# Kernel tuning notes

Hardware: AMD Instinct MI355X
Metric: run time of the kernel (lower is better)

Reference implementation:

```python
import jax, jax.numpy as jnp
import numpy as np
import math

# LLaMA-7B-style int8 attention (torch-int Int8LlamaAttention)
B, S, HID, NH, HD = 2, 1024, 4096, 32, 128
THETA = 10000.0
# per-tensor quantization scales (as produced by from_float)
S_IN, S_W, S_B = 0.02, 0.01, 0.1
S_Q, S_K, S_V, S_O = 0.05, 0.05, 0.05, 0.05


def _rope_tables(position_ids):
    inv_freq = 1.0 / (THETA ** (jnp.arange(0, HD, 2, dtype=jnp.float32) / HD))
    freqs = position_ids.astype(jnp.float32)[..., None] * inv_freq  # [B,S,HD//2]
    emb = jnp.concatenate([freqs, freqs], axis=-1)  # [B,S,HD]
    return jnp.cos(emb)[:, None], jnp.sin(emb)[:, None]  # [B,1,S,HD]


def _rotate_half(x):
    return jnp.concatenate([-x[..., HD // 2:], x[..., :HD // 2]], axis=-1)


def _quant_i8(x):
    return jnp.clip(jnp.round(x), -128, 127).astype(jnp.int8)


def _w8a8b8o8(x_i8, w_i8, b_i8, alpha, beta):
    # int8 GEMM with int32 accumulation, fused dequant-requant to int8
    acc = jnp.einsum('bsk,nk->bsn', x_i8.astype(jnp.int32), w_i8.astype(jnp.int32))
    return _quant_i8(acc.astype(jnp.float32) * alpha + b_i8.astype(jnp.float32) * beta)


def setup_inputs() -> dict:
    key = jax.random.key(0)
    ks = jax.random.split(key, 9)
    ri8 = lambda k, shp: jax.random.randint(k, shp, -127, 128, dtype=jnp.int8)
    return {
        'hidden_states': jax.random.normal(ks[0], (B, S, HID), jnp.float32),
        'position_ids': jnp.broadcast_to(jnp.arange(S, dtype=jnp.int32), (B, S)),
        'w_q': ri8(ks[1], (HID, HID)),
        'w_k': ri8(ks[2], (HID, HID)),
        'w_v': ri8(ks[3], (HID, HID)),
        'w_o': ri8(ks[4], (HID, HID)),
        'b_q': ri8(ks[5], (HID,)),
        'b_k': ri8(ks[6], (HID,)),
        'b_v': ri8(ks[7], (HID,)),
        'b_o': jax.random.normal(ks[8], (HID,), jnp.float32) * 0.01,
    }


def reference(hidden_states, position_ids, w_q, w_k, w_v, w_o, b_q, b_k, b_v, b_o):
    # quantize activations, run int8 q/k/v projections (W8A8B8O8Linear)
    x_i8 = _quant_i8(hidden_states / S_IN)
    q = _w8a8b8o8(x_i8, w_q, b_q, S_IN * S_W / S_Q, S_B / S_Q)
    k = _w8a8b8o8(x_i8, w_k, b_k, S_IN * S_W / S_K, S_B / S_K)
    v = _w8a8b8o8(x_i8, w_v, b_v, S_IN * S_W / S_V, S_B / S_V)
    to_heads = lambda t: t.reshape(B, S, NH, HD).transpose(0, 2, 1, 3)  # [B,NH,S,HD]
    q, k, v = to_heads(q), to_heads(k), to_heads(v)
    # RoPE applied on dequantized int8 values, requantized for the int8 qk bmm
    cos, sin = _rope_tables(position_ids)
    qf, kf = q.astype(jnp.float32), k.astype(jnp.float32)
    q_i8 = _quant_i8(qf * cos + _rotate_half(qf) * sin)
    k_i8 = _quant_i8(kf * cos + _rotate_half(kf) * sin)
    # BMM_S8T_S8N_F32T: int8 QK^T -> fp32 with scale s_q*s_k, then /sqrt(d)
    attn = jnp.einsum('bhsd,bhtd->bhst', q_i8.astype(jnp.int32), k_i8.astype(jnp.int32))
    attn = attn.astype(jnp.float32) * (S_Q * S_K) / math.sqrt(HD)
    # NOTE: source never applies the attention mask (`attn_weights = attn_weights`)
    p = jax.nn.softmax(attn, axis=-1)
    # probs quantized to int8 with scale 1/127 for BMM_S8T_S8N_S8T
    p_i8 = _quant_i8(p * 127.0)
    ctx = jnp.einsum('bhst,bhtd->bhsd', p_i8.astype(jnp.int32), v.astype(jnp.int32))
    ctx_i8 = _quant_i8(ctx.astype(jnp.float32) * ((1.0 / 127.0) * S_V / S_O))
    ctx_i8 = ctx_i8.transpose(0, 2, 1, 3).reshape(B, S, HID)
    # W8A8BFP32OFP32 o_proj: int8 GEMM, fp32 output + fp32 bias
    out = jnp.einsum('bsk,nk->bsn', ctx_i8.astype(jnp.int32), w_o.astype(jnp.int32))
    return out.astype(jnp.float32) * (S_O * S_W) + b_o
```

## Files before the change

### kernel.cpp

```cpp
#include <hip/hip_runtime.h>
#include <hip/hip_bf16.h>
#include <cstdint>
#include <cstddef>

typedef int v4i __attribute__((ext_vector_type(4)));

#define NH 32
#define HD 128
#define SEQ 1024
#define HID 4096
#define BB 2
#define BKB 128

__device__ __forceinline__ signed char quant_i8(float x) {
    float r = rintf(x);
    r = fminf(fmaxf(r, -128.0f), 127.0f);
    return (signed char)r;
}

#define GLOAD_LDS16(g, l) \
    __builtin_amdgcn_global_load_lds((const __attribute__((address_space(1))) void*)(g), \
                                     (__attribute__((address_space(3))) void*)(l), 16, 0, 0)

__global__ __launch_bounds__(256) void pack4_i8_kernel(
    const int* __restrict__ s0, const int* __restrict__ s1,
    const int* __restrict__ s2, const int* __restrict__ s3,
    signed char* __restrict__ d0, signed char* __restrict__ d1,
    signed char* __restrict__ d2, signed char* __restrict__ d3, int n4)
{
    int i = blockIdx.x * 256 + threadIdx.x;
    int which = i / n4;
    int idx = i - which * n4;
    const int* src = (which == 0) ? s0 : (which == 1) ? s1 : (which == 2) ? s2 : s3;
    signed char* dst = (which == 0) ? d0 : (which == 1) ? d1 : (which == 2) ? d2 : d3;
    int4 v = ((const int4*)src)[idx];
    char4 c;
    c.x = (signed char)v.x; c.y = (signed char)v.y;
    c.z = (signed char)v.z; c.w = (signed char)v.w;
    ((char4*)dst)[idx] = c;
}

__global__ __launch_bounds__(256) void quant_x_kernel(const float* __restrict__ src,
                                                      signed char* __restrict__ dst, int n4) {
    int i = blockIdx.x * 256 + threadIdx.x;
    if (i >= n4) return;
    float4 v = ((const float4*)src)[i];
    char4 c;
    c.x = quant_i8(v.x * 50.0f);
    c.y = quant_i8(v.y * 50.0f);
    c.z = quant_i8(v.z * 50.0f);
    c.w = quant_i8(v.w * 50.0f);
    ((char4*)dst)[i] = c;
}

template<int TM, bool F32OUT>
__device__ __forceinline__ void gemm_core(
    const signed char* __restrict__ A, const signed char* __restrict__ Bw,
    const void* __restrict__ bias, void* __restrict__ outp,
    int m0, int n0, int N, int K, float alpha, float beta)
{
    constexpr int MI = TM / 32;
    constexpr int PA = TM / 32;
    __shared__ __align__(16) signed char sA[TM * BKB];
    __shared__ __align__(16) signed char sB[128 * BKB];

    const int t    = threadIdx.x;
    const int w    = t >> 6;
    const int lane = t & 63;
    const int lm   = lane & 15;
    const int quad = lane >> 4;
    const int wm   = (w >> 1) * (TM / 2);
    const int wn   = (w & 1) * 64;

    int srowA[PA], skcA[PA];
    #pragma unroll
    for (int p = 0; p < PA; p++) {
        int si = t + 256 * p;
        int row = si >> 3;
        srowA[p] = row;
        skcA[p] = ((si & 7) - (row >> 1)) & 7;
    }
    int srowB[4], skcB[4];
    #pragma unroll
    for (int p = 0; p < 4; p++) {
        int si = t + 256 * p;
        int row = si >> 3;
        srowB[p] = row;
        skcB[p] = ((si & 7) - (row >> 1)) & 7;
    }

    v4i acc[MI][4] = {};

    for (int k0 = 0; k0 < K; k0 += BKB) {
        __syncthreads();
        #pragma unroll
        for (int p = 0; p < PA; p++) {
            const signed char* ga = A + (size_t)(m0 + srowA[p]) * K + k0 + skcA[p] * 16;
            GLOAD_LDS16(ga, sA + t * 16 + p * 4096);
        }
        #pragma unroll
        for (int p = 0; p < 4; p++) {
            const signed char* gb = Bw + (size_t)(n0 + srowB[p]) * K + k0 + skcB[p] * 16;
            GLOAD_LDS16(gb, sB + t * 16 + p * 4096);
        }
        __syncthreads();

        #pragma unroll
        for (int ks = 0; ks < 2; ks++) {
            v4i af[MI], bf[4];
            #pragma unroll
            for (int i = 0; i < MI; i++) {
                int row = wm + 16 * i + lm;
                int slot = (ks * 4 + quad + (lm >> 1)) & 7;
                af[i] = *(const v4i*)(sA + row * BKB + slot * 16);
            }
            #pragma unroll
            for (int j = 0; j < 4; j++) {
                int row = wn + 16 * j + lm;
                int slot = (ks * 4 + quad + (lm >> 1)) & 7;
                bf[j] = *(const v4i*)(sB + row * BKB + slot * 16);
            }
            #pragma unroll
            for (int i = 0; i < MI; i++)
                #pragma unroll
                for (int j = 0; j < 4; j++)
                    acc[i][j] = __builtin_amdgcn_mfma_i32_16x16x64_i8(af[i], bf[j], acc[i][j], 0, 0, 0);
        }
    }

    const int orow = quad * 4;
    #pragma unroll
    for (int i = 0; i < MI; i++) {
        #pragma unroll
        for (int j = 0; j < 4; j++) {
            #pragma unroll
            for (int r = 0; r < 4; r++) {
                int row = m0 + wm + 16 * i + orow + r;
                int col = n0 + wn + 16 * j + lm;
                float v = (float)acc[i][j][r];
                if (F32OUT) {
                    ((float*)outp)[(size_t)row * N + col] = v * alpha + ((const float*)bias)[col];
                } else {
                    float q = v * alpha + (float)((const int*)bias)[col] * beta;
                    ((signed char*)outp)[(size_t)row * N + col] = quant_i8(q);
                }
            }
        }
    }
}

__global__ __launch_bounds__(256) void gemm_qkv(
    const signed char* __restrict__ x8,
    const signed char* __restrict__ wq, const signed char* __restrict__ wk,
    const signed char* __restrict__ wv,
    const int* __restrict__ bq, const int* __restrict__ bk, const int* __restrict__ bv,
    signed char* __restrict__ q8, signed char* __restrict__ k8, signed char* __restrict__ v8)
{
    const int nblk = blockIdx.x;
    const int which = nblk >> 5;
    const int n0 = (nblk & 31) * 128;
    const int m0 = blockIdx.y * 128;
    const signed char* Bw = (which == 0) ? wq : (which == 1) ? wk : wv;
    const int* bias = (which == 0) ? bq : (which == 1) ? bk : bv;
    signed char* outp = (which == 0) ? q8 : (which == 1) ? k8 : v8;
    gemm_core<128, false>(x8, Bw, bias, outp, m0, n0, HID, HID, 0.004f, 2.0f);
}

__global__ __launch_bounds__(256) void gemm_o(
    const signed char* __restrict__ c8, const signed char* __restrict__ wo,
    const float* __restrict__ bo, float* __restrict__ outp)
{
    gemm_core<64, true>(c8, wo, bo, outp, blockIdx.y * 64, blockIdx.x * 128,
                        HID, HID, 0.0005f, 0.0f);
}

__global__ __launch_bounds__(128) void rope_kernel(
    const int* __restrict__ pos_ids, signed char* __restrict__ q,
    signed char* __restrict__ k, const signed char* __restrict__ v,
    signed char* __restrict__ vt)
{
    const int bid = blockIdx.x;
    const int sg = bid & 127;
    const int h  = (bid >> 7) & (NH - 1);
    const int b  = bid >> 12;
    const int d  = threadIdx.x;
    const int s0 = sg * 8;
    const int bh = b * NH + h;

    float inv = expf(-(float)(2 * (d & 63)) * (9.210340371976184f / 128.0f));

    float qd[8], qp[8], kd[8], kp[8];
    signed char vd[8];
    int pos[8];
    size_t base[8];
    #pragma unroll
    for (int i = 0; i < 8; i++) {
        int s = s0 + i;
        base[i] = ((size_t)(b * SEQ + s) * NH + h) * (size_t)HD;
        pos[i] = pos_ids[b * SEQ + s];
        qd[i] = (float)q[base[i] + d];
        qp[i] = (float)q[base[i] + (d ^ 64)];
        kd[i] = (float)k[base[i] + d];
        kp[i] = (float)k[base[i] + (d ^ 64)];
        vd[i] = v[base[i] + d];
    }
    __syncthreads();

    union { signed char c[8]; int2 i2; } vu;
    #pragma unroll
    for (int i = 0; i < 8; i++) {
        float freq = (float)pos[i] * inv;
        float cs = cosf(freq), sn = sinf(freq);
        float rotq = (d < 64) ? -qp[i] : qp[i];
        float rotk = (d < 64) ? -kp[i] : kp[i];
        q[base[i] + d] = quant_i8(qd[i] * cs + rotq * sn);
        k[base[i] + d] = quant_i8(kd[i] * cs + rotk * sn);
        vu.c[i] = vd[i];
    }
    *(int2*)(vt + ((size_t)(bh * HD + d)) * SEQ + s0) = vu.i2;
}

__global__ __launch_bounds__(256, 4) void attn_kernel(
    const signed char* __restrict__ q, const signed char* __restrict__ k,
    const signed char* __restrict__ vt, signed char* __restrict__ ctx)
{
    __shared__ __align__(16) signed char p8[16 * 1040];
    __shared__ float red[64];

    const int w    = threadIdx.x >> 6;
    const int lane = threadIdx.x & 63;
    const int bid  = blockIdx.x;
    const int mt   = bid & 63;
    const int bh   = bid >> 6;
    const int b    = bh >> 5, h = bh & 31;
    const int m0   = mt * 16;
    const int lm   = lane & 15;
    const int quad = lane >> 4;

    const float SCALE = 0.0025f / 11.313708498984761f;
    const float LOG2E = 1.4426950408889634f;

    const signed char* qbase = q + ((size_t)(b * SEQ + m0 + lm) * NH + h) * (size_t)HD + quad * 16;
    v4i qb0 = *(const v4i*)qbase;
    v4i qb1 = *(const v4i*)(qbase + 64);

    float vals[16][4];
    #pragma unroll
    for (int j = 0; j < 16; j++) {
        int t0 = w * 256 + j * 16;
        const signed char* kb = k + ((size_t)(b * SEQ + t0 + lm) * NH + h) * (size_t)HD + quad * 16;
        v4i a0 = *(const v4i*)kb;
        v4i a1 = *(const v4i*)(kb + 64);
        v4i acc = {};
        acc = __builtin_amdgcn_mfma_i32_16x16x64_i8(a0, qb0, acc, 0, 0, 0);
        acc = __builtin_amdgcn_mfma_i32_16x16x64_i8(a1, qb1, acc, 0, 0, 0);
        #pragma unroll
        for (int r = 0; r < 4; r++) vals[j][r] = (float)acc[r] * SCALE;
    }

    float mx = vals[0][0];
    #pragma unroll
    for (int j = 0; j < 16; j++)
        #pragma unroll
        for (int r = 0; r < 4; r++) mx = fmaxf(mx, vals[j][r]);
    mx = fmaxf(mx, __shfl_xor(mx, 16));
    mx = fmaxf(mx, __shfl_xor(mx, 32));
    if (lane < 16) red[w * 16 + lane] = mx;
    __syncthreads();
    mx = fmaxf(fmaxf(red[lm], red[16 + lm]), fmaxf(red[32 + lm], red[48 + lm]));

    float sum = 0.f;
    #pragma unroll
    for (int j = 0; j < 16; j++)
        #pragma unroll
        for (int r = 0; r < 4; r++) {
            vals[j][r] = exp2f((vals[j][r] - mx) * LOG2E);
            sum += vals[j][r];
        }
    sum += __shfl_xor(sum, 16);
    sum += __shfl_xor(sum, 32);
    __syncthreads();
    if (lane < 16) red[w * 16 + lane] = sum;
    __syncthreads();
    sum = (red[lm] + red[16 + lm]) + (red[32 + lm] + red[48 + lm]);
    float sf = 127.0f / sum;

    #pragma unroll
    for (int j = 0; j < 16; j++) {
        union { signed char cc[4]; int ii; } u;
        #pragma unroll
        for (int r = 0; r < 4; r++) u.cc[r] = quant_i8(vals[j][r] * sf);
        *(int*)(p8 + lm * 1040 + w * 256 + j * 16 + quad * 4) = u.ii;
    }
    __syncthreads();

    const int lkb = quad * 16;
    v4i accp[2] = {};
    for (int kk = 0; kk < SEQ; kk += 64) {
        v4i af = *(const v4i*)(p8 + lm * 1040 + kk + lkb);
        #pragma unroll
        for (int j = 0; j < 2; j++) {
            int col = w * 32 + j * 16;
            const signed char* vb = vt + ((size_t)(bh * HD + col + lm)) * (size_t)SEQ + kk + lkb;
            accp[j] = __builtin_amdgcn_mfma_i32_16x16x64_i8(af, *(const v4i*)vb, accp[j], 0, 0, 0);
        }
    }
    #pragma unroll
    for (int j = 0; j < 2; j++) {
        #pragma unroll
        for (int r = 0; r < 4; r++) {
            int row = quad * 4 + r;
            int col = w * 32 + j * 16 + lm;
            ctx[((size_t)(b * SEQ + m0 + row) * NH + h) * (size_t)HD + col] =
                quant_i8((float)accp[j][r] * (1.0f / 127.0f));
        }
    }
}

extern "C" void kernel_launch(void* const* d_in, const int* in_sizes, int n_in,
                              void* d_out, int out_size, void* d_ws, size_t ws_size,
                              hipStream_t stream)
{
    const float* hidden = (const float*)d_in[0];
    const int* pos_ids  = (const int*)d_in[1];
    const int* w_q = (const int*)d_in[2];
    const int* w_k = (const int*)d_in[3];
    const int* w_v = (const int*)d_in[4];
    const int* w_o = (const int*)d_in[5];
    const int* b_q = (const int*)d_in[6];
    const int* b_k = (const int*)d_in[7];
    const int* b_v = (const int*)d_in[8];
    const float* b_o = (const float*)d_in[9];
    float* out = (float*)d_out;

    char* ws = (char*)d_ws;
    const size_t WSZ = (size_t)HID * HID;
    signed char* wq8 = (signed char*)ws;
    signed char* wk8 = wq8 + WSZ;
    signed char* wv8 = wk8 + WSZ;
    signed char* wo8 = wv8 + WSZ;
    signed char* x8  = wo8 + WSZ;
    const size_t ASZ = (size_t)BB * SEQ * HID;
    signed char* q8  = x8 + ASZ;
    signed char* k8  = q8 + ASZ;
    signed char* v8  = k8 + ASZ;
    signed char* vt8 = v8 + ASZ;
    signed char* c8  = vt8 + ASZ;

    int wn4 = HID * HID / 4;
    pack4_i8_kernel<<<4 * wn4 / 256, 256, 0, stream>>>(w_q, w_k, w_v, w_o,
                                                       wq8, wk8, wv8, wo8, wn4);
    int xn4 = (int)(ASZ / 4);
    quant_x_kernel<<<xn4 / 256, 256, 0, stream>>>(hidden, x8, xn4);

    gemm_qkv<<<dim3(96, 16), 256, 0, stream>>>(x8, wq8, wk8, wv8, b_q, b_k, b_v,
                                               q8, k8, v8);

    rope_kernel<<<BB * NH * (SEQ / 8), 128, 0, stream>>>(pos_ids, q8, k8, v8, vt8);
    attn_kernel<<<BB * NH * (SEQ / 16), 256, 0, stream>>>(q8, k8, vt8, c8);

    gemm_o<<<dim3(32, 32), 256, 0, stream>>>(c8, wo8, b_o, out);
}
```

Baseline: 604.8 us.

## Double-buffer LDS in int8 GEMMs and process 32 query rows per attention block

```diff
diff --git a/kernel.cpp b/kernel.cpp
--- a/kernel.cpp
+++ b/kernel.cpp
@@ -53,84 +53,84 @@
     ((char4*)dst)[i] = c;
 }
 
-template<int TM, bool F32OUT>
-__device__ __forceinline__ void gemm_core(
+template<bool F32OUT>
+__device__ __forceinline__ void gemm_core_db(
     const signed char* __restrict__ A, const signed char* __restrict__ Bw,
     const void* __restrict__ bias, void* __restrict__ outp,
     int m0, int n0, int N, int K, float alpha, float beta)
 {
-    constexpr int MI = TM / 32;
-    constexpr int PA = TM / 32;
-    __shared__ __align__(16) signed char sA[TM * BKB];
-    __shared__ __align__(16) signed char sB[128 * BKB];
+    __shared__ __align__(16) signed char sA[2 * 128 * BKB];
+    __shared__ __align__(16) signed char sB[2 * 128 * BKB];
 
     const int t    = threadIdx.x;
     const int w    = t >> 6;
     const int lane = t & 63;
     const int lm   = lane & 15;
     const int quad = lane >> 4;
-    const int wm   = (w >> 1) * (TM / 2);
+    const int wm   = (w >> 1) * 64;
     const int wn   = (w & 1) * 64;
 
-    int srowA[PA], skcA[PA];
-    #pragma unroll
-    for (int p = 0; p < PA; p++) {
-        int si = t + 256 * p;
-        int row = si >> 3;
-        srowA[p] = row;
-        skcA[p] = ((si & 7) - (row >> 1)) & 7;
-    }
-    int srowB[4], skcB[4];
+    int srow[4], skc[4];
     #pragma unroll
     for (int p = 0; p < 4; p++) {
         int si = t + 256 * p;
         int row = si >> 3;
-        srowB[p] = row;
-        skcB[p] = ((si & 7) - (row >> 1)) & 7;
-    }
-
-    v4i acc[MI][4] = {};
-
+        srow[p] = row;
+        skc[p] = ((si & 7) - (row >> 1)) & 7;
+    }
+
+    v4i acc[4][4] = {};
+
+    #pragma unroll
+    for (int p = 0; p < 4; p++) {
+        GLOAD_LDS16(A  + (size_t)(m0 + srow[p]) * K + skc[p] * 16, sA + t * 16 + p * 4096);
+        GLOAD_LDS16(Bw + (size_t)(n0 + srow[p]) * K + skc[p] * 16, sB + t * 16 + p * 4096);
+    }
+
+    int buf = 0;
     for (int k0 = 0; k0 < K; k0 += BKB) {
         __syncthreads();
-        #pragma unroll
-        for (int p = 0; p < PA; p++) {
-            const signed char* ga = A + (size_t)(m0 + srowA[p]) * K + k0 + skcA[p] * 16;
-            GLOAD_LDS16(ga, sA + t * 16 + p * 4096);
-        }
-        #pragma unroll
-        for (int p = 0; p < 4; p++) {
-            const signed char* gb = Bw + (size_t)(n0 + srowB[p]) * K + k0 + skcB[p] * 16;
-            GLOAD_LDS16(gb, sB + t * 16 + p * 4096);
-        }
-        __syncthreads();
-
+
+        if (k0 + BKB < K) {
+            int nb = buf ^ 1;
+            #pragma unroll
+            for (int p = 0; p < 4; p++) {
+                GLOAD_LDS16(A  + (size_t)(m0 + srow[p]) * K + k0 + BKB + skc[p] * 16,
+                            sA + nb * 16384 + t * 16 + p * 4096);
+                GLOAD_LDS16(Bw + (size_t)(n0 + srow[p]) * K + k0 + BKB + skc[p] * 16,
+                            sB + nb * 16384 + t * 16 + p * 4096);
+            }
+        }
+
+        const signed char* pA = sA + buf * 16384;
+        const signed char* pB = sB + buf * 16384;
         #pragma unroll
         for (int ks = 0; ks < 2; ks++) {
-            v4i af[MI], bf[4];
-            #pragma unroll
-            for (int i = 0; i < MI; i++) {
+            v4i af[4], bf[4];
+            #pragma unroll
+            for (int i = 0; i < 4; i++) {
                 int row = wm + 16 * i + lm;
                 int slot = (ks * 4 + quad + (lm >> 1)) & 7;
-                af[i] = *(const v4i*)(sA + row * BKB + slot * 16);
+                af[i] = *(const v4i*)(pA + row * BKB + slot * 16);
             }
             #pragma unroll
             for (int j = 0; j < 4; j++) {
                 int row = wn + 16 * j + lm;
                 int slot = (ks * 4 + quad + (lm >> 1)) & 7;
-                bf[j] = *(const v4i*)(sB + row * BKB + slot * 16);
+                bf[j] = *(const v4i*)(pB + row * BKB + slot * 16);
             }
             #pragma unroll
-            for (int i = 0; i < MI; i++)
+            for (int i = 0; i < 4; i++)
                 #pragma unroll
                 for (int j = 0; j < 4; j++)
                     acc[i][j] = __builtin_amdgcn_mfma_i32_16x16x64_i8(af[i], bf[j], acc[i][j], 0, 0, 0);
         }
+        buf ^= 1;
     }
 
     const int orow = quad * 4;
     #pragma unroll
-    for (int i = 0; i < MI; i++) {
+    for (int i = 0; i < 4; i++) {
         #pragma unroll
         for (int j = 0; j < 4; j++) {
             #pragma unroll
@@ -163,15 +163,15 @@
     const signed char* Bw = (which == 0) ? wq : (which == 1) ? wk : wv;
     const int* bias = (which == 0) ? bq : (which == 1) ? bk : bv;
     signed char* outp = (which == 0) ? q8 : (which == 1) ? k8 : v8;
-    gemm_core<128, false>(x8, Bw, bias, outp, m0, n0, HID, HID, 0.004f, 2.0f);
+    gemm_core_db<false>(x8, Bw, bias, outp, m0, n0, HID, HID, 0.004f, 2.0f);
 }
 
 __global__ __launch_bounds__(256) void gemm_o(
     const signed char* __restrict__ c8, const signed char* __restrict__ wo,
     const float* __restrict__ bo, float* __restrict__ outp)
 {
-    gemm_core<64, true>(c8, wo, bo, outp, blockIdx.y * 64, blockIdx.x * 128,
-                        HID, HID, 0.0005f, 0.0f);
+    gemm_core_db<true>(c8, wo, bo, outp, blockIdx.y * 128, blockIdx.x * 128,
+                       HID, HID, 0.0005f, 0.0f);
 }
 
 __global__ __launch_bounds__(128) void rope_kernel(
@@ -220,89 +220,108 @@
     *(int2*)(vt + ((size_t)(bh * HD + d)) * SEQ + s0) = vu.i2;
 }
 
-__global__ __launch_bounds__(256, 4) void attn_kernel(
+__global__ __launch_bounds__(256) void attn_kernel(
     const signed char* __restrict__ q, const signed char* __restrict__ k,
     const signed char* __restrict__ vt, signed char* __restrict__ ctx)
 {
-    __shared__ __align__(16) signed char p8[16 * 1040];
-    __shared__ float red[64];
+    __shared__ __align__(16) signed char p8[32 * 1040];
+    __shared__ float red[128];
 
     const int w    = threadIdx.x >> 6;
     const int lane = threadIdx.x & 63;
     const int bid  = blockIdx.x;
-    const int mt   = bid & 63;
-    const int bh   = bid >> 6;
+    const int mt   = bid & 31;
+    const int bh   = bid >> 5;
     const int b    = bh >> 5, h = bh & 31;
-    const int m0   = mt * 16;
+    const int m0   = mt * 32;
     const int lm   = lane & 15;
     const int quad = lane >> 4;
 
     const float SCALE = 0.0025f / 11.313708498984761f;
     const float LOG2E = 1.4426950408889634f;
 
-    const signed char* qbase = q + ((size_t)(b * SEQ + m0 + lm) * NH + h) * (size_t)HD + quad * 16;
-    v4i qb0 = *(const v4i*)qbase;
-    v4i qb1 = *(const v4i*)(qbase + 64);
-
-    float vals[16][4];
+    const signed char* qb_base = q + ((size_t)(b * SEQ + m0 + lm) * NH + h) * (size_t)HD + quad * 16;
+    v4i qb0 = *(const v4i*)qb_base;
+    v4i qb1 = *(const v4i*)(qb_base + 64);
+    const signed char* qb_base2 = qb_base + (size_t)16 * NH * HD;
+    v4i qb2 = *(const v4i*)qb_base2;
+    v4i qb3 = *(const v4i*)(qb_base2 + 64);
+
+    float vals0[16][4], vals1[16][4];
     #pragma unroll
     for (int j = 0; j < 16; j++) {
         int t0 = w * 256 + j * 16;
         const signed char* kb = k + ((size_t)(b * SEQ + t0 + lm) * NH + h) * (size_t)HD + quad * 16;
         v4i a0 = *(const v4i*)kb;
         v4i a1 = *(const v4i*)(kb + 64);
-        v4i acc = {};
-        acc = __builtin_amdgcn_mfma_i32_16x16x64_i8(a0, qb0, acc, 0, 0, 0);
-        acc = __builtin_amdgcn_mfma_i32_16x16x64_i8(a1, qb1, acc, 0, 0, 0);
-        #pragma unroll
-        for (int r = 0; r < 4; r++) vals[j][r] = (float)acc[r] * SCALE;
-    }
-
-    float mx = vals[0][0];
+        v4i acc0 = {}, acc1 = {};
+        acc0 = __builtin_amdgcn_mfma_i32_16x16x64_i8(a0, qb0, acc0, 0, 0, 0);
+        acc0 = __builtin_amdgcn_mfma_i32_16x16x64_i8(a1, qb1, acc0, 0, 0, 0);
+        acc1 = __builtin_amdgcn_mfma_i32_16x16x64_i8(a0, qb2, acc1, 0, 0, 0);
+        acc1 = __builtin_amdgcn_mfma_i32_16x16x64_i8(a1, qb3, acc1, 0, 0, 0);
+        #pragma unroll
+        for (int r = 0; r < 4; r++) {
+            vals0[j][r] = (float)acc0[r] * SCALE;
+            vals1[j][r] = (float)acc1[r] * SCALE;
+        }
+    }
+
+    float mx0 = vals0[0][0], mx1 = vals1[0][0];
     #pragma unroll
     for (int j = 0; j < 16; j++)
         #pragma unroll
-        for (int r = 0; r < 4; r++) mx = fmaxf(mx, vals[j][r]);
-    mx = fmaxf(mx, __shfl_xor(mx, 16));
-    mx = fmaxf(mx, __shfl_xor(mx, 32));
-    if (lane < 16) red[w * 16 + lane] = mx;
-    __syncthreads();
-    mx = fmaxf(fmaxf(red[lm], red[16 + lm]), fmaxf(red[32 + lm], red[48 + lm]));
-
-    float sum = 0.f;
+        for (int r = 0; r < 4; r++) {
+            mx0 = fmaxf(mx0, vals0[j][r]);
+            mx1 = fmaxf(mx1, vals1[j][r]);
+        }
+    mx0 = fmaxf(mx0, __shfl_xor(mx0, 16)); mx0 = fmaxf(mx0, __shfl_xor(mx0, 32));
+    mx1 = fmaxf(mx1, __shfl_xor(mx1, 16)); mx1 = fmaxf(mx1, __shfl_xor(mx1, 32));
+    if (lane < 16) { red[w * 16 + lane] = mx0; red[64 + w * 16 + lane] = mx1; }
+    __syncthreads();
+    mx0 = fmaxf(fmaxf(red[lm], red[16 + lm]), fmaxf(red[32 + lm], red[48 + lm]));
+    mx1 = fmaxf(fmaxf(red[64 + lm], red[80 + lm]), fmaxf(red[96 + lm], red[112 + lm]));
+
+    float sum0 = 0.f, sum1 = 0.f;
     #pragma unroll
     for (int j = 0; j < 16; j++)
         #pragma unroll
         for (int r = 0; r < 4; r++) {
-            vals[j][r] = exp2f((vals[j][r] - mx) * LOG2E);
-            sum += vals[j][r];
-        }
-    sum += __shfl_xor(sum, 16);
-    sum += __shfl_xor(sum, 32);
-    __syncthreads();
-    if (lane < 16) red[w * 16 + lane] = sum;
-    __syncthreads();
-    sum = (red[lm] + red[16 + lm]) + (red[32 + lm] + red[48 + lm]);
-    float sf = 127.0f / sum;
+            vals0[j][r] = exp2f((vals0[j][r] - mx0) * LOG2E); sum0 += vals0[j][r];
+            vals1[j][r] = exp2f((vals1[j][r] - mx1) * LOG2E); sum1 += vals1[j][r];
+        }
+    sum0 += __shfl_xor(sum0, 16); sum0 += __shfl_xor(sum0, 32);
+    sum1 += __shfl_xor(sum1, 16); sum1 += __shfl_xor(sum1, 32);
+    __syncthreads();
+    if (lane < 16) { red[w * 16 + lane] = sum0; red[64 + w * 16 + lane] = sum1; }
+    __syncthreads();
+    sum0 = (red[lm] + red[16 + lm]) + (red[32 + lm] + red[48 + lm]);
+    sum1 = (red[64 + lm] + red[80 + lm]) + (red[96 + lm] + red[112 + lm]);
+    float sf0 = 127.0f / sum0, sf1 = 127.0f / sum1;
 
     #pragma unroll
     for (int j = 0; j < 16; j++) {
-        union { signed char cc[4]; int ii; } u;
-        #pragma unroll
-        for (int r = 0; r < 4; r++) u.cc[r] = quant_i8(vals[j][r] * sf);
-        *(int*)(p8 + lm * 1040 + w * 256 + j * 16 + quad * 4) = u.ii;
+        union { signed char cc[4]; int ii; } u0, u1;
+        #pragma unroll
+        for (int r = 0; r < 4; r++) {
+            u0.cc[r] = quant_i8(vals0[j][r] * sf0);
+            u1.cc[r] = quant_i8(vals1[j][r] * sf1);
+        }
+        *(int*)(p8 + lm * 1040 + w * 256 + j * 16 + quad * 4) = u0.ii;
+        *(int*)(p8 + (16 + lm) * 1040 + w * 256 + j * 16 + quad * 4) = u1.ii;
     }
     __syncthreads();
 
     const int lkb = quad * 16;
-    v4i accp[2] = {};
+    v4i accp0[2] = {}, accp1[2] = {};
     for (int kk = 0; kk < SEQ; kk += 64) {
-        v4i af = *(const v4i*)(p8 + lm * 1040 + kk + lkb);
+        v4i af0 = *(const v4i*)(p8 + lm * 1040 + kk + lkb);
+        v4i af1 = *(const v4i*)(p8 + (16 + lm) * 1040 + kk + lkb);
         #pragma unroll
         for (int j = 0; j < 2; j++) {
             int col = w * 32 + j * 16;
-            const signed char* vb = vt + ((size_t)(bh * HD + col + lm)) * (size_t)SEQ + kk + lkb;
-            accp[j] = __builtin_amdgcn_mfma_i32_16x16x64_i8(af, *(const v4i*)vb, accp[j], 0, 0, 0);
+            v4i vb = *(const v4i*)(vt + ((size_t)(bh * HD + col + lm)) * (size_t)SEQ + kk + lkb);
+            accp0[j] = __builtin_amdgcn_mfma_i32_16x16x64_i8(af0, vb, accp0[j], 0, 0, 0);
+            accp1[j] = __builtin_amdgcn_mfma_i32_16x16x64_i8(af1, vb, accp1[j], 0, 0, 0);
         }
     }
     #pragma unroll
@@ -312,7 +331,9 @@
             int row = quad * 4 + r;
             int col = w * 32 + j * 16 + lm;
             ctx[((size_t)(b * SEQ + m0 + row) * NH + h) * (size_t)HD + col] =
-                quant_i8((float)accp[j][r] * (1.0f / 127.0f));
+                quant_i8((float)accp0[j][r] * (1.0f / 127.0f));
+            ctx[((size_t)(b * SEQ + m0 + 16 + row) * NH + h) * (size_t)HD + col] =
+                quant_i8((float)accp1[j][r] * (1.0f / 127.0f));
         }
     }
 }
@@ -357,7 +378,7 @@
                                                q8, k8, v8);
 
     rope_kernel<<<BB * NH * (SEQ / 8), 128, 0, stream>>>(pos_ids, q8, k8, v8, vt8);
-    attn_kernel<<<BB * NH * (SEQ / 16), 256, 0, stream>>>(q8, k8, vt8, c8);
-
-    gemm_o<<<dim3(32, 32), 256, 0, stream>>>(c8, wo8, b_o, out);
-}
+    attn_kernel<<<BB * NH * (SEQ / 32), 256, 0, stream>>>(q8, k8, vt8, c8);
+
+    gemm_o<<<dim3(32, 16), 256, 0, stream>>>(c8, wo8, b_o, out);
+}
```

Result: faster. 544.0 us (-10.0%).
